# Kernel optimization log

Measured on AMD Instinct MI355X. Metric: run time of the kernel, lower is better.

The kernel has to match this reference:

```python
import jax, jax.numpy as jnp
import numpy as np

K = 1024
H = 16

def setup_inputs() -> dict:
    key = jax.random.key(0)
    ks = jax.random.split(key, 6)
    s = 1.0 / np.sqrt(K)
    return {
        "x": jax.random.normal(ks[0], (2, 2048, K), dtype=jnp.float32),
        "Wq": jax.random.uniform(ks[1], (K, K), jnp.float32, -s, s),
        "Wk": jax.random.uniform(ks[2], (K, K), jnp.float32, -s, s),
        "Wv": jax.random.uniform(ks[3], (K, K), jnp.float32, -s, s),
        "Wu": jax.random.uniform(ks[4], (K, K), jnp.float32, -s, s),
        "bu": jax.random.uniform(ks[5], (K,), jnp.float32, -s, s),
    }

def reference(x, Wq, Wk, Wv, Wu, bu):
    b, t, k = x.shape
    hd = k // H  # head dim = 64
    scale = jnp.asarray(k, x.dtype) ** 0.25  # Bloem-style: scale q and k each by k^(1/4)
    # nn.Linear(bias=False): y = x @ W.T
    q = (jnp.einsum('btk,ok->bto', x, Wq) / scale).reshape(b, t, H, hd)
    kk = (jnp.einsum('btk,ok->bto', x, Wk) / scale).reshape(b, t, H, hd)
    v = jnp.einsum('btk,ok->bto', x, Wv).reshape(b, t, H, hd)
    dot = jnp.einsum('bthd,bshd->bhts', q, kk)  # [b,h,t,t]
    att = jax.nn.softmax(dot, axis=-1)
    out = jnp.einsum('bhts,bshd->bthd', att, v).reshape(b, t, k)
    return jnp.einsum('btk,ok->bto', out, Wu) + bu
```

## Files before the change

kernel.cpp:

```cpp
#include <hip/hip_runtime.h>

typedef __bf16 bf16;
typedef bf16  bf16x8 __attribute__((ext_vector_type(8)));
typedef bf16  bf16x4 __attribute__((ext_vector_type(4)));
typedef float f32x4  __attribute__((ext_vector_type(4)));
typedef unsigned int u32x2 __attribute__((ext_vector_type(2)));
typedef unsigned int u32x4 __attribute__((ext_vector_type(4)));

#define MFMA16(a, b, c) __builtin_amdgcn_mfma_f32_16x16x32_bf16((a), (b), (c), 0, 0, 0)
#define AS1 __attribute__((address_space(1)))
#define AS3 __attribute__((address_space(3)))

__device__ __forceinline__ void gld_lds16(const bf16* g, bf16* l) {
    __builtin_amdgcn_global_load_lds((AS1 void*)(g), (AS3 void*)(l), 16, 0, 0);
}


__global__ __launch_bounds__(256) void cvt_all(const float* __restrict__ x,
                                               const float* __restrict__ Wq, const float* __restrict__ Wk,
                                               const float* __restrict__ Wv, const float* __restrict__ Wu,
                                               bf16* ox, bf16* oq, bf16* ok, bf16* ov, bf16* ou,
                                               float sq, float sk) {
    int bid = blockIdx.x;
    const float* src; bf16* dst; float sc; int base;
    if (bid < 4096) { src = x; dst = ox; sc = 1.0f; base = bid; }
    else {
        int w = (bid - 4096) >> 10; base = (bid - 4096) & 1023;
        switch (w) {
            case 0:  src = Wq; dst = oq; sc = sq;   break;
            case 1:  src = Wk; dst = ok; sc = sk;   break;
            case 2:  src = Wv; dst = ov; sc = 1.0f; break;
            default: src = Wu; dst = ou; sc = 1.0f; break;
        }
    }
    int idx = (base * 256 + threadIdx.x) * 4;
    float4 v = *(const float4*)(src + idx);
    bf16x4 o;
    o[0] = (bf16)(v.x * sc); o[1] = (bf16)(v.y * sc);
    o[2] = (bf16)(v.z * sc); o[3] = (bf16)(v.w * sc);
    *(bf16x4*)(dst + idx) = o;
}

__device__ __forceinline__ void gemm_core(const bf16* __restrict__ A, const bf16* __restrict__ B,
                                          int mBase, int nBase, bf16* As, bf16* Bs,
                                          f32x4 acc[4][4]) {
    const int tid = threadIdx.x;
    const int wave = tid >> 6, lane = tid & 63;
    const int g = lane >> 4, lr = lane & 15;
    const int wm = (wave & 1) << 6, wn = (wave >> 1) << 6;
    const int q = lane >> 2;
    const int cswz = ((lane & 3) ^ ((lane >> 3) & 3)) << 3;
    const int pcs  = (g ^ ((lr >> 1) & 3)) << 3;

    const int rb0 = wave << 4, rb1 = rb0 + 64;
    const bf16* a0 = A + (size_t)(mBase + rb0 + q) * 1024 + cswz;
    const bf16* a1 = A + (size_t)(mBase + rb1 + q) * 1024 + cswz;
    const bf16* b0 = B + (size_t)(nBase + rb0 + q) * 1024 + cswz;
    const bf16* b1 = B + (size_t)(nBase + rb1 + q) * 1024 + cswz;

    gld_lds16(a0, As + rb0 * 32);
    gld_lds16(a1, As + rb1 * 32);
    gld_lds16(b0, Bs + rb0 * 32);
    gld_lds16(b1, Bs + rb1 * 32);
    __syncthreads();

    for (int k0 = 0; k0 < 1024; k0 += 32) {
        const int cur = (k0 >> 5) & 1;
        bf16* Asc = As + cur * (128 * 32);
        bf16* Bsc = Bs + cur * (128 * 32);
        if (k0 + 32 < 1024) {
            bf16* Asn = As + (cur ^ 1) * (128 * 32);
            bf16* Bsn = Bs + (cur ^ 1) * (128 * 32);
            gld_lds16(a0 + k0 + 32, Asn + rb0 * 32);
            gld_lds16(a1 + k0 + 32, Asn + rb1 * 32);
            gld_lds16(b0 + k0 + 32, Bsn + rb0 * 32);
            gld_lds16(b1 + k0 + 32, Bsn + rb1 * 32);
        }

        bf16x8 af[4], bfr[4];
#pragma unroll
        for (int i = 0; i < 4; i++)
            af[i] = *(const bf16x8*)&Asc[(wm + (i << 4) + lr) * 32 + pcs];
#pragma unroll
        for (int j = 0; j < 4; j++)
            bfr[j] = *(const bf16x8*)&Bsc[(wn + (j << 4) + lr) * 32 + pcs];
#pragma unroll
        for (int i = 0; i < 4; i++)
#pragma unroll
            for (int j = 0; j < 4; j++)
                acc[i][j] = MFMA16(af[i], bfr[j], acc[i][j]);

        __syncthreads();
    }
}

__global__ __launch_bounds__(256) void gemm_qkv(const bf16* __restrict__ X,
                                                const bf16* __restrict__ Wqk,
                                                const bf16* __restrict__ Wv,
                                                bf16* __restrict__ Qo, bf16* __restrict__ Ko,
                                                bf16* __restrict__ Vto) {
    __shared__ bf16 As[2][128 * 32];
    __shared__ bf16 Bs[2][128 * 32];
    const int tid = threadIdx.x;
    const int wave = tid >> 6, lane = tid & 63;
    const int g = lane >> 4, lr = lane & 15;
    const int wm = (wave & 1) << 6, wn = (wave >> 1) << 6;
    const int my = blockIdx.y;
    const bool qk = (my < 16);

    const bf16* Ap = qk ? Wqk : X;
    const bf16* Bp = qk ? X   : Wv;
    const int mBase = qk ? my * 128 : blockIdx.x * 128;
    const int nBase = qk ? blockIdx.x * 128 : (my - 16) * 128;

    f32x4 acc[4][4] = {};
    gemm_core(Ap, Bp, mBase, nBase, &As[0][0], &Bs[0][0], acc);

    if (qk) {
#pragma unroll
        for (int i = 0; i < 4; i++) {
            int m0 = mBase + wm + (i << 4) + (g << 2);
            bf16* dst = (m0 >> 10) ? Ko : Qo;
            int feat = m0 & 1023;
            int h = feat >> 6, d = feat & 63;
#pragma unroll
            for (int j = 0; j < 4; j++) {
                int t = nBase + wn + (j << 4) + lr;
                int b = t >> 11, tl = t & 2047;
                bf16x4 v;
#pragma unroll
                for (int r = 0; r < 4; r++) v[r] = (bf16)acc[i][j][r];
                *(bf16x4*)&dst[(((size_t)((b << 4) + h) * 2048 + tl) << 6) + d] = v;
            }
        }
    } else {
#pragma unroll
        for (int i = 0; i < 4; i++) {
            int t0 = mBase + wm + (i << 4) + (g << 2);
            int b = t0 >> 11, tl = t0 & 2047;
#pragma unroll
            for (int j = 0; j < 4; j++) {
                int o = nBase + wn + (j << 4) + lr;
                int h = o >> 6, d = o & 63;
                bf16x4 v;
#pragma unroll
                for (int r = 0; r < 4; r++) v[r] = (bf16)acc[i][j][r];
                *(bf16x4*)&Vto[((size_t)(((b << 4) + h) << 6) + d) * 2048 + tl] = v;
            }
        }
    }
}

__global__ __launch_bounds__(256) void gemm_out(const bf16* __restrict__ Wu, const bf16* __restrict__ A,
                                                const float* __restrict__ bias, float* __restrict__ out) {
    __shared__ bf16 As[2][128 * 32];
    __shared__ bf16 Bs[2][128 * 32];
    const int tid = threadIdx.x;
    const int wave = tid >> 6, lane = tid & 63;
    const int g = lane >> 4, lr = lane & 15;
    const int wm = (wave & 1) << 6, wn = (wave >> 1) << 6;
    const int mBase = blockIdx.y * 128, nBase = blockIdx.x * 128;

    f32x4 acc[4][4] = {};
    gemm_core(Wu, A, mBase, nBase, &As[0][0], &Bs[0][0], acc);

#pragma unroll
    for (int i = 0; i < 4; i++) {
        int o = mBase + wm + (i << 4) + (g << 2);
        float4 bv = *(const float4*)&bias[o];
#pragma unroll
        for (int j = 0; j < 4; j++) {
            int t = nBase + wn + (j << 4) + lr;
            float4 v;
            v.x = acc[i][j][0] + bv.x;
            v.y = acc[i][j][1] + bv.y;
            v.z = acc[i][j][2] + bv.z;
            v.w = acc[i][j][3] + bv.w;
            *(float4*)&out[((size_t)t << 10) + o] = v;
        }
    }
}

__global__ __launch_bounds__(256, 4) void attn(const bf16* __restrict__ Q, const bf16* __restrict__ Kt,
                                               const bf16* __restrict__ Vt, bf16* __restrict__ O) {
    __shared__ bf16 Qs[2][64][32];
    __shared__ bf16 Ks[2][128][32];
    __shared__ bf16 Vs[4][64][32];

    const int tid = threadIdx.x;
    const int wave = tid >> 6, lane = tid & 63;
    const int g = lane >> 4, lr = lane & 15;
    const int q = lane >> 2;
    const int cswz = ((lane & 3) ^ ((lane >> 3) & 3)) << 3;
    const int pcs  = (g ^ ((lr >> 1) & 3)) << 3;
    const int pair = wave >> 1;
    const int shalf = wave & 1;

    const int bid = blockIdx.x;
    const int bh = ((bid & 7) << 2) | (bid >> 8);
    const int qBase = ((bid >> 3) & 31) << 6;

    const bf16* Qg = Q + ((size_t)bh * 2048 + qBase) * 64;
    const bf16* Kg = Kt + (size_t)bh * 2048 * 64;
    const bf16* Vg = Vt + (size_t)bh * 64 * 2048;

#pragma unroll
    for (int i = 0; i < 2; i++) {
        int bi = (wave << 1) + i;
        int p = bi >> 2, rb = (bi & 3) << 4;
        gld_lds16(Qg + (rb + q) * 64 + (p << 5) + cswz, &Qs[p][rb][0]);
    }
    __syncthreads();

    bf16x8 qf[2][2];
#pragma unroll
    for (int ks = 0; ks < 2; ks++)
#pragma unroll
        for (int tt = 0; tt < 2; tt++)
            qf[ks][tt] = *(const bf16x8*)&Qs[ks][(pair << 5) + (tt << 4) + lr][pcs];

    bf16x8 ones;
#pragma unroll
    for (int i = 0; i < 8; i++) ones[i] = (bf16)1.0f;

    f32x4 oacc[2][4] = {};
    f32x4 oaccL[2] = {};

    for (int s0 = 0; s0 < 2048; s0 += 128) {
        __syncthreads();
#pragma unroll
        for (int i = 0; i < 4; i++) {
            int bi = (wave << 2) + i;
            {
                int p = bi >> 3, rb = (bi & 7) << 4;
                gld_lds16(Kg + (size_t)(s0 + rb + q) * 64 + (p << 5) + cswz, &Ks[p][rb][0]);
            }
            {
                int p = bi >> 2, rb = (bi & 3) << 4;
                gld_lds16(Vg + (size_t)(rb + q) * 2048 + s0 + (p << 5) + cswz, &Vs[p][rb][0]);
            }
        }
        __syncthreads();

#pragma unroll
        for (int sblk = 0; sblk < 2; sblk++) {
            f32x4 sacc[2][2] = {};
#pragma unroll
            for (int ks = 0; ks < 2; ks++)
#pragma unroll
                for (int isub = 0; isub < 2; isub++) {
                    bf16x8 kf = *(const bf16x8*)
                        &Ks[ks][(shalf << 6) + (sblk << 5) + (isub << 4) + lr][pcs];
                    sacc[isub][0] = MFMA16(kf, qf[ks][0], sacc[isub][0]);
                    sacc[isub][1] = MFMA16(kf, qf[ks][1], sacc[isub][1]);
                }
            bf16x8 pf[2];
#pragma unroll
            for (int tt = 0; tt < 2; tt++) {
                bf16x4 e0, e1;
#pragma unroll
                for (int r = 0; r < 4; r++) {
                    e0[r] = (bf16)__builtin_amdgcn_exp2f(sacc[0][tt][r]);
                    e1[r] = (bf16)__builtin_amdgcn_exp2f(sacc[1][tt][r]);
                }
                u32x2 a = __builtin_bit_cast(u32x2, e0);
                u32x2 b = __builtin_bit_cast(u32x2, e1);
                u32x2 t0  = __builtin_amdgcn_permlane32_swap(a.x, b.x, false, false);
                u32x2 w02 = __builtin_amdgcn_permlane16_swap(t0.x, t0.y, false, false);
                u32x2 t1  = __builtin_amdgcn_permlane32_swap(a.y, b.y, false, false);
                u32x2 w13 = __builtin_amdgcn_permlane16_swap(t1.x, t1.y, false, false);
                u32x4 w = {w02.x, w13.x, w02.y, w13.y};
                pf[tt] = __builtin_bit_cast(bf16x8, w);
            }
#pragma unroll
            for (int jd = 0; jd < 4; jd++) {
                bf16x8 vf = *(const bf16x8*)&Vs[(shalf << 1) + sblk][(jd << 4) + lr][pcs];
                oacc[0][jd] = MFMA16(pf[0], vf, oacc[0][jd]);
                oacc[1][jd] = MFMA16(pf[1], vf, oacc[1][jd]);
            }
            oaccL[0] = MFMA16(pf[0], ones, oaccL[0]);
            oaccL[1] = MFMA16(pf[1], ones, oaccL[1]);
        }
    }

    __syncthreads();
    float* Odump = (float*)&Ks[0][0][0];
    float* Ldump = (float*)&Vs[0][0][0];
    if (shalf == 1) {
#pragma unroll
        for (int tt = 0; tt < 2; tt++) {
#pragma unroll
            for (int jd = 0; jd < 4; jd++)
                *(f32x4*)&Odump[(pair << 11) + (((tt << 2) + jd) << 8) + (lane << 2)] = oacc[tt][jd];
            *(f32x4*)&Ldump[(pair << 9) + (tt << 8) + (lane << 2)] = oaccL[tt];
        }
    }
    __syncthreads();
    if (shalf == 0) {
        const int b = bh >> 4, h = bh & 15;
#pragma unroll
        for (int tt = 0; tt < 2; tt++) {
            f32x4 Lp = *(const f32x4*)&Ldump[(pair << 9) + (tt << 8) + (lane << 2)];
            f32x4 Ls = oaccL[tt] + Lp;
            float linv[4];
#pragma unroll
            for (int r = 0; r < 4; r++) linv[r] = 1.0f / Ls[r];
#pragma unroll
            for (int jd = 0; jd < 4; jd++) {
                f32x4 Op = *(const f32x4*)&Odump[(pair << 11) + (((tt << 2) + jd) << 8) + (lane << 2)];
                f32x4 v = oacc[tt][jd] + Op;
#pragma unroll
                for (int r = 0; r < 4; r++) {
                    int t = qBase + (pair << 5) + (tt << 4) + (g << 2) + r;
                    int col = (h << 6) + (jd << 4) + lr;
                    O[(((size_t)(b * 2048 + t)) << 10) + col] = (bf16)(v[r] * linv[r]);
                }
            }
        }
    }
}

extern "C" void kernel_launch(void* const* d_in, const int* in_sizes, int n_in,
                              void* d_out, int out_size, void* d_ws, size_t ws_size,
                              hipStream_t stream) {
    const float* x  = (const float*)d_in[0];
    const float* Wq = (const float*)d_in[1];
    const float* Wk = (const float*)d_in[2];
    const float* Wv = (const float*)d_in[3];
    const float* Wu = (const float*)d_in[4];
    const float* bu = (const float*)d_in[5];
    float* out = (float*)d_out;

    char* ws = (char*)d_ws;
    bf16* xbf  = (bf16*)(ws);
    bf16* wqbf = (bf16*)(ws + ((size_t)8  << 20));
    bf16* wkbf = (bf16*)(ws + ((size_t)10 << 20));
    bf16* wvbf = (bf16*)(ws + ((size_t)12 << 20));
    bf16* wubf = (bf16*)(ws + ((size_t)14 << 20));
    bf16* Qb   = (bf16*)(ws + ((size_t)16 << 20));
    bf16* Kb   = (bf16*)(ws + ((size_t)24 << 20));
    bf16* Vtb  = (bf16*)(ws + ((size_t)32 << 20));
    bf16* attnO = xbf;

    const float iscale_k = 0.17677669529663687f;
    const float iscale_q = 0.25503540109f;

    cvt_all<<<8192, 256, 0, stream>>>(x, Wq, Wk, Wv, Wu, xbf, wqbf, wkbf, wvbf, wubf,
                                      iscale_q, iscale_k);

    gemm_qkv<<<dim3(32, 24), 256, 0, stream>>>(xbf, wqbf, wvbf, Qb, Kb, Vtb);
    attn<<<dim3(1024), 256, 0, stream>>>(Qb, Kb, Vtb, attnO);
    gemm_out<<<dim3(32, 8), 256, 0, stream>>>(wubf, attnO, bu, out);
}
```

Baseline: 185.0 us.

## Enlarge QKV GEMM to 256x256 tiles with 512 threads and interleaved prefetch

Rewrites the fused QKV projection GEMM to use 256x256 output tiles with 8 waves per block, so 192 blocks run instead of 768. Each wave computes a 128x64 sub-tile in two halves, and the next K-slice's A and B loads are issued between them with barriers and MFMA priority raised. The larger tiles raise operand reuse and cut global/LDS traffic per FLOP. In exchange, 192 blocks may underfill the 256 CUs and each thread holds more accumulator registers.

```diff
diff --git a/kernel.cpp b/kernel.cpp
--- a/kernel.cpp
+++ b/kernel.cpp
@@ -94,39 +94,96 @@
     }
 }
 
-__global__ __launch_bounds__(256) void gemm_qkv(const bf16* __restrict__ X,
-                                                const bf16* __restrict__ Wqk,
-                                                const bf16* __restrict__ Wv,
-                                                bf16* __restrict__ Qo, bf16* __restrict__ Ko,
-                                                bf16* __restrict__ Vto) {
-    __shared__ bf16 As[2][128 * 32];
-    __shared__ bf16 Bs[2][128 * 32];
+__device__ __forceinline__ void stage_tile16(const bf16* G, int k0, bf16* Ls,
+                                             int wave, int q, int cswz) {
+#pragma unroll
+    for (int c = 0; c < 2; c++) {
+        int rb = c * 8 + wave;
+        gld_lds16(G + (size_t)(rb * 16 + q) * 1024 + k0 + cswz, Ls + rb * 16 * 32);
+    }
+}
+
+__global__ __launch_bounds__(512, 2) void gemm_qkv(const bf16* __restrict__ X,
+                                                   const bf16* __restrict__ Wqk,
+                                                   const bf16* __restrict__ Wv,
+                                                   bf16* __restrict__ Qo, bf16* __restrict__ Ko,
+                                                   bf16* __restrict__ Vto) {
+    __shared__ bf16 As[2][256][32];
+    __shared__ bf16 Bs[2][256][32];
     const int tid = threadIdx.x;
     const int wave = tid >> 6, lane = tid & 63;
     const int g = lane >> 4, lr = lane & 15;
-    const int wm = (wave & 1) << 6, wn = (wave >> 1) << 6;
-    const int my = blockIdx.y;
-    const bool qk = (my < 16);
-
-    const bf16* Ap = qk ? Wqk : X;
-    const bf16* Bp = qk ? X   : Wv;
-    const int mBase = qk ? my * 128 : blockIdx.x * 128;
-    const int nBase = qk ? blockIdx.x * 128 : (my - 16) * 128;
-
-    f32x4 acc[4][4] = {};
-    gemm_core(Ap, Bp, mBase, nBase, &As[0][0], &Bs[0][0], acc);
+    const int q = lane >> 2;
+    const int cswz = ((lane & 3) ^ ((lane >> 3) & 3)) << 3;
+    const int pcs  = (g ^ ((lr >> 1) & 3)) << 3;
+    const int wm = wave >> 2, wn = wave & 3;
+
+    const int bid = blockIdx.x;
+    const bool qk = bid < 128;
+    int mBase, nBase;
+    const bf16 *Ap, *Bp;
+    if (qk) { mBase = (bid >> 4) << 8; nBase = (bid & 15) << 8; Ap = Wqk; Bp = X; }
+    else    { int v = bid - 128; mBase = (v >> 2) << 8; nBase = (v & 3) << 8; Ap = X; Bp = Wv; }
+
+    const bf16* Ag = Ap + (size_t)mBase * 1024;
+    const bf16* Bg = Bp + (size_t)nBase * 1024;
+
+    f32x4 acc[8][4] = {};
+
+    stage_tile16(Ag, 0, &As[0][0][0], wave, q, cswz);
+    stage_tile16(Bg, 0, &Bs[0][0][0], wave, q, cswz);
+    __syncthreads();
+
+    for (int t = 0; t < 32; t++) {
+        const int k0 = t << 5;
+        bf16* Ac = &As[t & 1][0][0];
+        bf16* Bc = &Bs[t & 1][0][0];
+        const bool pre = (t < 31);
+
+        bf16x8 bfr[4], af[4];
+#pragma unroll
+        for (int j = 0; j < 4; j++)
+            bfr[j] = *(const bf16x8*)&Bc[(wn * 64 + (j << 4) + lr) * 32 + pcs];
+#pragma unroll
+        for (int i = 0; i < 4; i++)
+            af[i] = *(const bf16x8*)&Ac[(wm * 128 + (i << 4) + lr) * 32 + pcs];
+        if (pre) stage_tile16(Ag, k0 + 32, &As[(t & 1) ^ 1][0][0], wave, q, cswz);
+        __builtin_amdgcn_s_barrier();
+        __builtin_amdgcn_s_setprio(1);
+#pragma unroll
+        for (int i = 0; i < 4; i++)
+#pragma unroll
+            for (int j = 0; j < 4; j++)
+                acc[i][j] = MFMA16(af[i], bfr[j], acc[i][j]);
+        __builtin_amdgcn_s_setprio(0);
+
+#pragma unroll
+        for (int i = 0; i < 4; i++)
+            af[i] = *(const bf16x8*)&Ac[(wm * 128 + 64 + (i << 4) + lr) * 32 + pcs];
+        if (pre) stage_tile16(Bg, k0 + 32, &Bs[(t & 1) ^ 1][0][0], wave, q, cswz);
+        __builtin_amdgcn_s_barrier();
+        __builtin_amdgcn_s_setprio(1);
+#pragma unroll
+        for (int i = 0; i < 4; i++)
+#pragma unroll
+            for (int j = 0; j < 4; j++)
+                acc[4 + i][j] = MFMA16(af[i], bfr[j], acc[4 + i][j]);
+        __builtin_amdgcn_s_setprio(0);
+
+        __syncthreads();
+    }
 
     if (qk) {
 #pragma unroll
-        for (int i = 0; i < 4; i++) {
-            int m0 = mBase + wm + (i << 4) + (g << 2);
+        for (int i = 0; i < 8; i++) {
+            int m0 = mBase + wm * 128 + (i << 4) + (g << 2);
             bf16* dst = (m0 >> 10) ? Ko : Qo;
             int feat = m0 & 1023;
             int h = feat >> 6, d = feat & 63;
 #pragma unroll
             for (int j = 0; j < 4; j++) {
-                int t = nBase + wn + (j << 4) + lr;
-                int b = t >> 11, tl = t & 2047;
+                int tt = nBase + wn * 64 + (j << 4) + lr;
+                int b = tt >> 11, tl = tt & 2047;
                 bf16x4 v;
 #pragma unroll
                 for (int r = 0; r < 4; r++) v[r] = (bf16)acc[i][j][r];
@@ -135,12 +192,12 @@
         }
     } else {
 #pragma unroll
-        for (int i = 0; i < 4; i++) {
-            int t0 = mBase + wm + (i << 4) + (g << 2);
+        for (int i = 0; i < 8; i++) {
+            int t0 = mBase + wm * 128 + (i << 4) + (g << 2);
             int b = t0 >> 11, tl = t0 & 2047;
 #pragma unroll
             for (int j = 0; j < 4; j++) {
-                int o = nBase + wn + (j << 4) + lr;
+                int o = nBase + wn * 64 + (j << 4) + lr;
                 int h = o >> 6, d = o & 63;
                 bf16x4 v;
 #pragma unroll
@@ -348,7 +405,7 @@
     cvt_all<<<8192, 256, 0, stream>>>(x, Wq, Wk, Wv, Wu, xbf, wqbf, wkbf, wvbf, wubf,
                                       iscale_q, iscale_k);
 
-    gemm_qkv<<<dim3(32, 24), 256, 0, stream>>>(xbf, wqbf, wvbf, Qb, Kb, Vtb);
+    gemm_qkv<<<dim3(192), 512, 0, stream>>>(xbf, wqbf, wvbf, Qb, Kb, Vtb);
     attn<<<dim3(1024), 256, 0, stream>>>(Qb, Kb, Vtb, attnO);
     gemm_out<<<dim3(32, 8), 256, 0, stream>>>(wubf, attnO, bu, out);
 }
```

After: 185.0 us. Within noise of the previous version (-0.0%).
